# Kernel optimization log

Measured on AMD Instinct MI355X. Metric: run time of the kernel, lower is better.

Reference implementation:

```python
import jax, jax.numpy as jnp
import numpy as np

EMBED = 768
DIM = 800          # embed + 32 gender features
IN_C = 1024
GRID = 32          # img_size // patch_size(=1)
LN_EPS = 1e-5      # torch nn.LayerNorm default


def setup_inputs() -> dict:
    key = jax.random.key(0)
    ks = jax.random.split(key, 8)
    B = 32
    x = jax.random.normal(ks[0], (B, IN_C, GRID, GRID), dtype=jnp.float32)
    gender_encode = jax.random.normal(ks[1], (B, 32), dtype=jnp.float32)
    # PatchEmbed 1x1 conv (acts as per-pixel linear) + LayerNorm params
    conv_w = jax.random.normal(ks[2], (EMBED, IN_C), dtype=jnp.float32) * (IN_C ** -0.5)
    conv_b = jnp.zeros((EMBED,), dtype=jnp.float32)
    ln_g = jnp.ones((EMBED,), dtype=jnp.float32)
    ln_b = jnp.zeros((EMBED,), dtype=jnp.float32)
    cls_token = jax.random.normal(ks[3], (1, 1, EMBED), dtype=jnp.float32) * 0.02
    # Attention qkv linear (bias=True); proj is never used in the forward path
    qkv_w = jax.random.normal(ks[4], (3 * DIM, DIM), dtype=jnp.float32) * (DIM ** -0.5)
    qkv_b = jnp.zeros((3 * DIM,), dtype=jnp.float32)
    return {
        "x": x, "gender_encode": gender_encode,
        "conv_w": conv_w, "conv_b": conv_b,
        "ln_g": ln_g, "ln_b": ln_b,
        "cls_token": cls_token,
        "qkv_w": qkv_w, "qkv_b": qkv_b,
    }


def _forward(x, gender_encode, conv_w, conv_b, ln_g, ln_b, cls_token, qkv_w, qkv_b):
    B = x.shape[0]
    # PatchEmbed: 1x1 conv stride 1 == per-pixel linear; flatten(2).transpose(1,2)
    p = jnp.einsum('bchw,oc->bhwo', x, conv_w) + conv_b        # [B,32,32,768]
    p = p.reshape(B, GRID * GRID, EMBED)                        # [B,1024,768]
    mu = jnp.mean(p, axis=-1, keepdims=True)
    var = jnp.mean((p - mu) ** 2, axis=-1, keepdims=True)
    p = (p - mu) * jax.lax.rsqrt(var + LN_EPS) * ln_g + ln_b
    # prepend cls token, concat broadcast gender features
    cls = jnp.broadcast_to(cls_token, (B, 1, EMBED))
    t = jnp.concatenate([cls, p], axis=1)                       # [B,1025,768]
    g = jnp.broadcast_to(gender_encode[:, None, :], (B, t.shape[1], 32))
    t = jnp.concatenate([t, g], axis=2)                         # [B,1025,800]
    # Attention (note: self.norm / proj / v are unused in the original forward)
    qkv = t @ qkv_w.T + qkv_b                                   # [B,1025,2400]
    q = qkv[..., 0:DIM]
    k = qkv[..., DIM:2 * DIM]
    scale = DIM ** -0.5
    # only the cls-query row is ever used -> compute just that row
    scores = jnp.einsum('bc,bnc->bn', q[:, 0], k) * scale       # [B,1025]
    attn_cls = jax.nn.softmax(scores[:, 1:], axis=-1)           # [B,1024]
    return attn_cls.reshape(B, 1, GRID, GRID)


def reference(x, gender_encode, conv_w, conv_b, ln_g, ln_b, cls_token, qkv_w, qkv_b):
    return _forward(x, gender_encode, conv_w, conv_b, ln_g, ln_b, cls_token, qkv_w, qkv_b)
```

## Files before the change

kernel.cpp:

```cpp
#include <hip/hip_runtime.h>
#include <hip/hip_bf16.h>

#define EMBED 768
#define DIMQ  800
#define INC   1024
#define NPIX  1024

typedef __bf16 bf16_t;
typedef __bf16 bf16x8 __attribute__((ext_vector_type(8)));
typedef __bf16 bf16x2 __attribute__((ext_vector_type(2)));
typedef float  f32x4  __attribute__((ext_vector_type(4)));

#define GLD_LDS(gp, lp) __builtin_amdgcn_global_load_lds( \
    (const __attribute__((address_space(1))) void*)(gp),  \
    (__attribute__((address_space(3))) void*)(lp), 16, 0, 0)

__global__ __launch_bounds__(256)
void k_prep(const float* __restrict__ w, bf16_t* __restrict__ cw,
            const float* __restrict__ qkv_w, const float* __restrict__ qkv_b,
            const float* __restrict__ cls, const float* __restrict__ gender,
            float* __restrict__ q0b) {
    const int bi = blockIdx.x;
    const int t  = threadIdx.x;
    if (bi < 200) {
        const int wv = t >> 6, tl = t & 63;
        const int i = bi * 4 + wv;
        const float* row = qkv_w + (size_t)i * DIMQ;
        float ps = 0.f;
        for (int j = tl; j < EMBED; j += 64) ps += row[j] * cls[j];
#pragma unroll
        for (int off = 1; off < 64; off <<= 1) ps += __shfl_xor(ps, off, 64);
        if (tl < 32) {
            float g = 0.f;
#pragma unroll
            for (int j = 0; j < 32; ++j) g += row[EMBED + j] * gender[tl * 32 + j];
            q0b[tl * DIMQ + i] = ps + g + qkv_b[i];
        }
    } else {
        const int i = (bi - 200) * 256 + t;
        const int n = i >> 10, k = i & 1023;
        const int s = (k >> 3) & 7;
        const int src_k = (k & ~63) | (((s ^ (n & 7)) & 7) << 3) | (k & 7);
        cw[i] = (bf16_t)w[(size_t)n * 1024 + src_k];
    }
}

__global__ __launch_bounds__(256)
void k_u(const float* __restrict__ qkv_w, const float* __restrict__ q0b,
         const float* __restrict__ ln_g, float* __restrict__ u) {
    __shared__ float q0s[DIMQ];
    __shared__ float sh[8][33];
    int t = threadIdx.x;
    int b  = blockIdx.x / 24;
    int j0 = (blockIdx.x % 24) * 32;
    for (int i = t; i < DIMQ; i += 256) q0s[i] = q0b[b * DIMQ + i];
    __syncthreads();
    int j_l = t & 31, os = t >> 5;
    const float* wk = qkv_w + (size_t)DIMQ * DIMQ;
    const float* wp = wk + (size_t)(os * 100) * DIMQ + j0 + j_l;
    float acc = 0.f;
#pragma unroll 4
    for (int i = 0; i < 100; ++i) acc += wp[(size_t)i * DIMQ] * q0s[os * 100 + i];
    sh[os][j_l] = acc;
    __syncthreads();
    if (t < 32) {
        float s = 0.f;
#pragma unroll
        for (int o = 0; o < 8; ++o) s += sh[o][t];
        u[b * EMBED + j0 + t] = s * ln_g[j0 + t];
    }
}

__global__ __launch_bounds__(256, 3)
void k_main(const float* __restrict__ x, const bf16_t* __restrict__ cw,
            const float* __restrict__ conv_b, const float* __restrict__ u,
            float* __restrict__ partial) {
    __shared__ __align__(1024) unsigned char smem[32768 + 3072];

    const int tid = threadIdx.x;
    const int bi = blockIdx.x;
    const int x8 = bi & 7;
    const int s  = bi >> 3;
    const int nt = s % 6;
    const int mt = (s / 6) * 8 + x8;
    const int b  = mt >> 3;
    const int gm = mt * 128;
    const int gmm = gm & 1023;
    const int gn = nt * 128;

    const int wv = tid >> 6;
    const int l  = tid & 63;
    const int lr = l >> 3;
    const int lc = l & 7;

    const int lane = l;
    const int col  = lane & 15;
    const int quad = lane >> 4;
    const int wm   = (wv >> 1) * 64;
    const int wn   = (wv & 1) * 64;

    bf16_t* A = (bf16_t*)smem;
    bf16_t* B = (bf16_t*)(smem + 16384);

    const int m4 = (tid >> 3) * 4;
    const float* xsrc = x + ((size_t)(b * 1024 + (tid & 7) * 8) * 1024) + gmm + m4;

    f32x4 C[4][4] = {};

    for (int kt = 0; kt < 16; ++kt) {
        const int ko = kt * 64;
#pragma unroll
        for (int p = 0; p < 4; ++p) {
            const int r = p * 32 + wv * 8 + lr;
            GLD_LDS(cw + (size_t)(gn + r) * 1024 + ko + lc * 8, B + (p * 32 + wv * 8) * 64);
        }
        f32x4 f4[8];
#pragma unroll
        for (int kk = 0; kk < 8; ++kk)
            f4[kk] = *(const f32x4*)(xsrc + (size_t)(ko + kk) * 1024);
#pragma unroll
        for (int mm = 0; mm < 4; ++mm) {
            bf16x8 w8;
#pragma unroll
            for (int kk = 0; kk < 8; ++kk) w8[kk] = (bf16_t)f4[kk][mm];
            const int r  = m4 + mm;
            const int ss = (tid & 7) ^ (r & 7);
            *(bf16x8*)(A + r * 64 + ss * 8) = w8;
        }
        __syncthreads();
#pragma unroll
        for (int ks = 0; ks < 2; ++ks) {
            bf16x8 af[4], bg[4];
#pragma unroll
            for (int mi = 0; mi < 4; ++mi) {
                const int r  = wm + mi * 16 + col;
                const int ph = (ks * 4 + quad) ^ (r & 7);
                af[mi] = *(const bf16x8*)(A + r * 64 + ph * 8);
            }
#pragma unroll
            for (int ni = 0; ni < 4; ++ni) {
                const int r  = wn + ni * 16 + col;
                const int ph = (ks * 4 + quad) ^ (r & 7);
                bg[ni] = *(const bf16x8*)(B + r * 64 + ph * 8);
            }
#pragma unroll
            for (int mi = 0; mi < 4; ++mi)
#pragma unroll
                for (int ni = 0; ni < 4; ++ni)
                    C[mi][ni] = __builtin_amdgcn_mfma_f32_16x16x32_bf16(af[mi], bg[ni], C[mi][ni], 0, 0, 0);
        }
        __syncthreads();
    }

    float cb[4], uv[4];
#pragma unroll
    for (int ni = 0; ni < 4; ++ni) {
        const int og = gn + wn + ni * 16 + col;
        cb[ni] = conv_b[og];
        uv[ni] = u[b * EMBED + og];
    }
    float* part = (float*)(smem + 32768);
#pragma unroll
    for (int mi = 0; mi < 4; ++mi)
#pragma unroll
        for (int r = 0; r < 4; ++r) {
            float a = 0.f, sq = 0.f, d = 0.f;
#pragma unroll
            for (int ni = 0; ni < 4; ++ni) {
                float v = C[mi][ni][r] + cb[ni];
                a += v; sq += v * v; d += v * uv[ni];
            }
#pragma unroll
            for (int off = 1; off < 16; off <<= 1) {
                a  += __shfl_xor(a, off, 64);
                sq += __shfl_xor(sq, off, 64);
                d  += __shfl_xor(d, off, 64);
            }
            if (col == 0) {
                const int row = wm + mi * 16 + quad * 4 + r;
                float* pp = part + ((wv & 1) * 128 + row) * 3;
                pp[0] = a; pp[1] = sq; pp[2] = d;
            }
        }
    __syncthreads();
    if (tid < 128) {
        const float* p0 = part + tid * 3;
        const float* p1 = part + (128 + tid) * 3;
        const size_t pix = (size_t)gm + tid;
        partial[(size_t)(0 * 6 + nt) * 32768 + pix] = p0[0] + p1[0];
        partial[(size_t)(1 * 6 + nt) * 32768 + pix] = p0[1] + p1[1];
        partial[(size_t)(2 * 6 + nt) * 32768 + pix] = p0[2] + p1[2];
    }
}

__global__ __launch_bounds__(1024)
void k_final(const float* __restrict__ partial, const float* __restrict__ u,
             float* __restrict__ out) {
    __shared__ float red[16];
    __shared__ float bc[3];
    const int b = blockIdx.x, t = threadIdx.x;
    const int lane = t & 63, wid = t >> 6;

    float pu = (t < EMBED) ? u[b * EMBED + t] : 0.f;
#pragma unroll
    for (int off = 1; off < 64; off <<= 1) pu += __shfl_xor(pu, off, 64);
    if (lane == 0) red[wid] = pu;
    __syncthreads();
    if (t == 0) { float s = 0.f; for (int i = 0; i < 16; ++i) s += red[i]; bc[0] = s; }
    __syncthreads();
    const float Su = bc[0];

    const size_t m = (size_t)b * 1024 + t;
    float S1 = 0.f, S2 = 0.f, S3 = 0.f;
#pragma unroll
    for (int nt = 0; nt < 6; ++nt) {
        S1 += partial[(size_t)(0 * 6 + nt) * 32768 + m];
        S2 += partial[(size_t)(1 * 6 + nt) * 32768 + m];
        S3 += partial[(size_t)(2 * 6 + nt) * 32768 + m];
    }
    const float mu  = S1 * (1.f / 768.f);
    const float var = S2 * (1.f / 768.f) - mu * mu;
    const float sc  = 0.035355339059327376f * (S3 - mu * Su) * rsqrtf(var + 1e-5f);

    float mx = sc;
#pragma unroll
    for (int off = 1; off < 64; off <<= 1) mx = fmaxf(mx, __shfl_xor(mx, off, 64));
    if (lane == 0) red[wid] = mx;
    __syncthreads();
    if (t == 0) { float mm = -1e30f; for (int i = 0; i < 16; ++i) mm = fmaxf(mm, red[i]); bc[1] = mm; }
    __syncthreads();
    const float e = __expf(sc - bc[1]);
    float ss = e;
#pragma unroll
    for (int off = 1; off < 64; off <<= 1) ss += __shfl_xor(ss, off, 64);
    __syncthreads();
    if (lane == 0) red[wid] = ss;
    __syncthreads();
    if (t == 0) { float s = 0.f; for (int i = 0; i < 16; ++i) s += red[i]; bc[2] = s; }
    __syncthreads();
    out[m] = e / bc[2];
}

extern "C" void kernel_launch(void* const* d_in, const int* in_sizes, int n_in,
                              void* d_out, int out_size, void* d_ws, size_t ws_size,
                              hipStream_t stream) {
    const float* x      = (const float*)d_in[0];
    const float* gender = (const float*)d_in[1];
    const float* conv_w = (const float*)d_in[2];
    const float* conv_b = (const float*)d_in[3];
    const float* ln_g   = (const float*)d_in[4];
    const float* cls    = (const float*)d_in[6];
    const float* qkv_w  = (const float*)d_in[7];
    const float* qkv_b  = (const float*)d_in[8];
    float* out = (float*)d_out;

    char* ws = (char*)d_ws;
    bf16_t* cw      = (bf16_t*)ws;
    float*  q0b     = (float*)(ws + 1572864);
    float*  u       = (float*)(ws + 1675264);
    float*  partial = (float*)(ws + 1773568);

    hipLaunchKernelGGL(k_prep,  dim3(3272),  dim3(256),  0, stream,
                       conv_w, cw, qkv_w, qkv_b, cls, gender, q0b);
    hipLaunchKernelGGL(k_u,     dim3(768),   dim3(256),  0, stream, qkv_w, q0b, ln_g, u);
    hipLaunchKernelGGL(k_main,  dim3(1536),  dim3(256),  0, stream, x, cw, conv_b, u, partial);
    hipLaunchKernelGGL(k_final, dim3(32),    dim3(1024), 0, stream, partial, u, out);
}
```

Before: 314.5 us.

## Software-pipeline conv GEMM with double-buffered weight tiles and register-prefetched x

Restructures the k_main main loop so that the bf16 weight tile for step t+2 is fetched asynchronously into one of two LDS buffers while step t computes. The fp32 x tile for the next step is also prefetched into registers before it is converted to bf16 and written to A. The per-iteration __syncthreads pair is replaced by explicit s_waitcnt and barrier sequences, so global latency should overlap with the MFMA work. In exchange, LDS use grows to 48KB per block and register pressure rises from the prefetched x values, which may limit occupancy. The epilogue reduction buffer now reuses the start of the LDS region.

Result: faster. 302.1 us (-3.9%).

```diff
diff --git a/kernel.cpp b/kernel.cpp
--- a/kernel.cpp
+++ b/kernel.cpp
@@ -75,7 +75,7 @@
 void k_main(const float* __restrict__ x, const bf16_t* __restrict__ cw,
             const float* __restrict__ conv_b, const float* __restrict__ u,
             float* __restrict__ partial) {
-    __shared__ __align__(1024) unsigned char smem[32768 + 3072];
+    __shared__ __align__(1024) unsigned char smem[49152];
 
     const int tid = threadIdx.x;
     const int bi = blockIdx.x;
@@ -93,41 +93,66 @@
     const int lr = l >> 3;
     const int lc = l & 7;
 
-    const int lane = l;
-    const int col  = lane & 15;
-    const int quad = lane >> 4;
+    const int col  = l & 15;
+    const int quad = l >> 4;
     const int wm   = (wv >> 1) * 64;
     const int wn   = (wv & 1) * 64;
 
-    bf16_t* A = (bf16_t*)smem;
-    bf16_t* B = (bf16_t*)(smem + 16384);
+    bf16_t* A  = (bf16_t*)smem;
+    bf16_t* B0 = (bf16_t*)(smem + 16384);
+    bf16_t* B1 = (bf16_t*)(smem + 32768);
 
     const int m4 = (tid >> 3) * 4;
     const float* xsrc = x + ((size_t)(b * 1024 + (tid & 7) * 8) * 1024) + gmm + m4;
 
+    f32x4 f4[8];
     f32x4 C[4][4] = {};
 
-    for (int kt = 0; kt < 16; ++kt) {
-        const int ko = kt * 64;
-#pragma unroll
-        for (int p = 0; p < 4; ++p) {
-            const int r = p * 32 + wv * 8 + lr;
-            GLD_LDS(cw + (size_t)(gn + r) * 1024 + ko + lc * 8, B + (p * 32 + wv * 8) * 64);
-        }
-        f32x4 f4[8];
-#pragma unroll
-        for (int kk = 0; kk < 8; ++kk)
-            f4[kk] = *(const f32x4*)(xsrc + (size_t)(ko + kk) * 1024);
-#pragma unroll
-        for (int mm = 0; mm < 4; ++mm) {
-            bf16x8 w8;
-#pragma unroll
-            for (int kk = 0; kk < 8; ++kk) w8[kk] = (bf16_t)f4[kk][mm];
-            const int r  = m4 + mm;
-            const int ss = (tid & 7) ^ (r & 7);
-            *(bf16x8*)(A + r * 64 + ss * 8) = w8;
-        }
-        __syncthreads();
+#define LOADX(tt) do {                                                      \
+        _Pragma("unroll")                                                   \
+        for (int kk = 0; kk < 8; ++kk)                                      \
+            f4[kk] = *(const f32x4*)(xsrc + (size_t)((tt) * 64 + kk) * 1024); \
+    } while (0)
+
+#define WRITEA() do {                                        \
+        _Pragma("unroll")                                                   \
+        for (int mm = 0; mm < 4; ++mm) {                                    \
+            bf16x8 w8;                                                      \
+            _Pragma("unroll")                                               \
+            for (int kk = 0; kk < 8; ++kk) w8[kk] = (bf16_t)f4[kk][mm];     \
+            const int r  = m4 + mm;                                         \
+            const int ss = (tid & 7) ^ (r & 7);                             \
+            *(bf16x8*)(A + r * 64 + ss * 8) = w8;                           \
+        }                                                                   \
+    } while (0)
+
+#define GLDB(tt, dst) do {                                                  \
+        _Pragma("unroll")                                                   \
+        for (int p = 0; p < 4; ++p) {                                       \
+            const int r = p * 32 + wv * 8 + lr;                             \
+            GLD_LDS(cw + (size_t)(gn + r) * 1024 + (tt) * 64 + lc * 8,      \
+                    (dst) + (p * 32 + wv * 8) * 64);                        \
+        }                                                                   \
+    } while (0)
+
+#define WAIT_VM0()  asm volatile("s_waitcnt vmcnt(0)" ::: "memory")
+#define WAIT_LGKM0() asm volatile("s_waitcnt lgkmcnt(0)" ::: "memory")
+#define SBAR() do { __builtin_amdgcn_sched_barrier(0);                      \
+                    __builtin_amdgcn_s_barrier();                           \
+                    __builtin_amdgcn_sched_barrier(0); } while (0)
+
+    LOADX(0);
+    GLDB(0, B0);
+    GLDB(1, B1);
+    WAIT_VM0();
+    WRITEA();
+    LOADX(1);
+    WAIT_LGKM0();
+    SBAR();
+
+#pragma unroll 1
+    for (int t = 0; t < 16; ++t) {
+        bf16_t* Bb = (t & 1) ? B1 : B0;
 #pragma unroll
         for (int ks = 0; ks < 2; ++ks) {
             bf16x8 af[4], bg[4];
@@ -141,7 +166,7 @@
             for (int ni = 0; ni < 4; ++ni) {
                 const int r  = wn + ni * 16 + col;
                 const int ph = (ks * 4 + quad) ^ (r & 7);
-                bg[ni] = *(const bf16x8*)(B + r * 64 + ph * 8);
+                bg[ni] = *(const bf16x8*)(Bb + r * 64 + ph * 8);
             }
 #pragma unroll
             for (int mi = 0; mi < 4; ++mi)
@@ -149,9 +174,22 @@
                 for (int ni = 0; ni < 4; ++ni)
                     C[mi][ni] = __builtin_amdgcn_mfma_f32_16x16x32_bf16(af[mi], bg[ni], C[mi][ni], 0, 0, 0);
         }
-        __syncthreads();
-    }
-
+        if (t == 15) break;
+        SBAR();
+        WAIT_VM0();
+        WRITEA();
+        if (t < 14) {
+            GLDB(t + 2, Bb);
+            LOADX(t + 2);
+        }
+        WAIT_LGKM0();
+        SBAR();
+    }
+#undef LOADX
+#undef WRITEA
+#undef GLDB
+
+    SBAR();
     float cb[4], uv[4];
 #pragma unroll
     for (int ni = 0; ni < 4; ++ni) {
@@ -159,7 +197,7 @@
         cb[ni] = conv_b[og];
         uv[ni] = u[b * EMBED + og];
     }
-    float* part = (float*)(smem + 32768);
+    float* part = (float*)smem;
 #pragma unroll
     for (int mi = 0; mi < 4; ++mi)
 #pragma unroll
```
